# Kernel tuning notes

Hardware: AMD Instinct MI355X
Metric: run time of the kernel (lower is better)

The kernel has to match this reference:

```python
import jax, jax.numpy as jnp
import numpy as np

DIM = 256   # state dimension
T = 8192    # number of time steps
B = 32      # batch of initial conditions
DT = 0.01   # time-grid spacing


def make_A(dim):
    # Faithful to MagnusLadder.__init__: diag=-0.1, superdiag=+0.5, subdiag=-0.5
    A = np.zeros((dim, dim), dtype=np.float32)
    np.fill_diagonal(A, -0.1)
    idx = np.arange(dim - 1)
    A[idx, idx + 1] = 0.5
    A[idx + 1, idx] = -0.5
    return jnp.asarray(A)


def setup_inputs() -> dict:
    key = jax.random.key(0)
    x0 = jax.random.normal(key, (DIM, B), dtype=jnp.float32)
    t = jnp.arange(T, dtype=jnp.float32) * DT  # uniform time grid, dt = DT
    A = make_A(DIM)
    return {"t": t, "x0": x0, "A": A}


def reference(t, x0, A):
    dt = t[1] - t[0]
    expAdt = jax.scipy.linalg.expm(A * dt)  # [dim, dim]

    def step(x, _):
        x = expAdt @ x  # [dim, B]
        return x, x

    _, traj = jax.lax.scan(step, x0, None, length=T - 1)  # [T-1, dim, B]
    return jnp.concatenate([x0[None], traj], axis=0)       # [T, dim, B]
```

## Files before the change

### kernel.cpp

```cpp
#include <hip/hip_runtime.h>
#include <hip/hip_bf16.h>


#define DIMN 256
#define BB   32
#define TSTEPS 8192
#define KT   32
#define DTF  0.01f

typedef __attribute__((ext_vector_type(8))) short bf16x8;
typedef __attribute__((ext_vector_type(4))) float f32x4;

static __device__ __forceinline__ short f2bf(float f) {
    union { __hip_bfloat16 h; short s; } u;
    u.h = __float2bfloat16(f);
    return u.s;
}

__global__ __launch_bounds__(256) void k1_prep(const float* __restrict__ x0,
                                               unsigned short* __restrict__ vfold,
                                               float* __restrict__ yr,
                                               float* __restrict__ yi) {
    const float PI257 = (float)(3.14159265358979323846 / 257.0);
    const float S257  = sqrtf(2.0f / 257.0f);
    const int g = blockIdx.x;
    const int t = threadIdx.x;

    __shared__ float x0s[256 * 32];
    __shared__ float ve[256], vo[256];
    __shared__ float psr[8][32], psi[8][32];

    if (g < 256) {
        const int j = g, J = j >> 1, p = j & 1, m = t;
        const int n = ((j + 1) * (m + 1)) % 514;
        const float v = S257 * sinf((float)n * PI257);
        float sgn;
        if (p == 0) sgn = (J & 1) ? -1.f : 1.f;
        else        sgn = (J & 1) ?  1.f : -1.f;
        vfold[p * 32768 + J * 256 + m] = (unsigned short)f2bf(sgn * v);
    } else {
        const int m = g - 256;
        for (int idx = t; idx < 256 * 32; idx += 256) x0s[idx] = x0[idx];
        const int n = ((m + 1) * (t + 1)) % 514;
        const float v = S257 * sinf((float)n * PI257);
        const int j = t;
        float veJ = 0.f, voJ = 0.f;
        if ((j & 1) == 0) veJ = ((j & 3) == 0) ? v : -v;
        else              voJ = ((j & 3) == 3) ? v : -v;
        ve[j] = veJ; vo[j] = voJ;
        __syncthreads();
        const int b = t & 31, jg = t >> 5;
        float sr = 0.f, si = 0.f;
#pragma unroll
        for (int jj2 = 0; jj2 < 32; ++jj2) {
            const int jj = jg * 32 + jj2;
            sr += ve[jj] * x0s[jj * 32 + b];
            si += vo[jj] * x0s[jj * 32 + b];
        }
        psr[jg][b] = sr; psi[jg][b] = si;
        __syncthreads();
        if (t < 32) {
            float asr = 0.f, asi = 0.f;
#pragma unroll
            for (int q = 0; q < 8; ++q) { asr += psr[q][t]; asi += psi[q][t]; }
            yr[m * 32 + t] = asr;
            yi[m * 32 + t] = asi;
        }
    }
}

__global__ __launch_bounds__(512, 2) void k2_main(const unsigned short* __restrict__ vfold,
                                                  const float* __restrict__ yr,
                                                  const float* __restrict__ yi,
                                                  float* __restrict__ out) {
    __shared__ unsigned short ubuf[2][2][2][8192];
    const float PI257   = (float)(3.14159265358979323846 / 257.0);
    const float INV2PI  = (float)(1.0 / (2.0 * 3.14159265358979323846));
    const int tid  = threadIdx.x;
    const int lane = tid & 63;
    const int wave = tid >> 6;
    const int k0   = blockIdx.x * KT;

    const int bA   = tid & 15;
    const int mblk = tid >> 4;
    const int m0   = mblk << 3;

    float threv[8], yrv0[8], yiv0[8], yrv1[8], yiv1[8];
#pragma unroll
    for (int i = 0; i < 8; ++i) {
        const int m = m0 + i;
        const float lam = cosf((float)(m + 1) * PI257);
        threv[i] = DTF * lam * INV2PI;
        yrv0[i] = yr[m * 32 + bA];       yiv0[i] = yi[m * 32 + bA];
        yrv1[i] = yr[m * 32 + bA + 16];  yiv1[i] = yi[m * 32 + bA + 16];
    }
    const int ksA = m0 >> 5, gA2 = (m0 >> 3) & 3;
    const int wOff0 = bA * 256        + (((ksA ^ (bA & 7)))        << 3) + (gA2 << 6);
    const int wOff1 = (bA + 16) * 256 + (((ksA ^ ((bA + 16) & 7))) << 3) + (gA2 << 6);

    const int p  = wave & 1;
    const int nt = (wave >> 1) & 1;
    const int rh = wave >> 2;
    const int rA = lane & 15;
    const int gA = lane >> 4;
    bf16x8 afr[4][8];
#pragma unroll
    for (int rt = 0; rt < 4; ++rt) {
        const unsigned short* arow =
            vfold + p * 32768 + (rh * 64 + rt * 16 + rA) * 256 + gA * 8;
#pragma unroll
        for (int ks = 0; ks < 8; ++ks)
            afr[rt][ks] = *reinterpret_cast<const bf16x8*>(arow + ks * 32);
    }
    const int brd   = nt * 16 + rA;
    const int h     = brd & 7;
    const int rbase = brd * 256 + (gA << 6);

    float dec = expf(-0.001f * (float)k0);
    const float decr = expf(-0.001f);

    for (int r = 0; r < KT / 2; ++r) {
        const int d = r & 1;
#pragma unroll
        for (int kw = 0; kw < 2; ++kw) {
            const float kf = (float)(k0 + 2 * r + kw);
            bf16x8 vur0, vui0, vur1, vui1;
#pragma unroll
            for (int i = 0; i < 8; ++i) {
                const float ang = kf * threv[i];
                const float fr  = ang - floorf(ang);
                const float c   = __builtin_amdgcn_cosf(fr);
                const float s   = __builtin_amdgcn_sinf(fr);
                vur0[i] = f2bf(c * yrv0[i] - s * yiv0[i]);
                vui0[i] = f2bf(c * yiv0[i] + s * yrv0[i]);
                vur1[i] = f2bf(c * yrv1[i] - s * yiv1[i]);
                vui1[i] = f2bf(c * yiv1[i] + s * yrv1[i]);
            }
            *reinterpret_cast<bf16x8*>(&ubuf[d][kw][0][wOff0]) = vur0;
            *reinterpret_cast<bf16x8*>(&ubuf[d][kw][1][wOff0]) = vui0;
            *reinterpret_cast<bf16x8*>(&ubuf[d][kw][0][wOff1]) = vur1;
            *reinterpret_cast<bf16x8*>(&ubuf[d][kw][1][wOff1]) = vui1;
        }
        __syncthreads();

#pragma unroll
        for (int kw = 0; kw < 2; ++kw) {
            const unsigned short* up = &ubuf[d][kw][p][0];
            float* outk = out + (size_t)(k0 + 2 * r + kw) * 8192;
            f32x4 acc[4];
#pragma unroll
            for (int rt = 0; rt < 4; ++rt) acc[rt] = (f32x4){0.f, 0.f, 0.f, 0.f};
#pragma unroll
            for (int ks = 0; ks < 8; ++ks) {
                const bf16x8 bfr =
                    *reinterpret_cast<const bf16x8*>(up + rbase + ((ks ^ h) << 3));
#pragma unroll
                for (int rt = 0; rt < 4; ++rt)
                    acc[rt] = __builtin_amdgcn_mfma_f32_16x16x32_bf16(
                        afr[rt][ks], bfr, acc[rt], 0, 0, 0);
            }
#pragma unroll
            for (int rt = 0; rt < 4; ++rt) {
#pragma unroll
                for (int q = 0; q < 4; ++q) {
                    const int j = 2 * (rh * 64 + rt * 16 + gA * 4 + q) + p;
                    outk[j * 32 + brd] = acc[rt][q] * dec;
                }
            }
            dec *= decr;
        }
    }
}

extern "C" void kernel_launch(void* const* d_in, const int* in_sizes, int n_in,
                              void* d_out, int out_size, void* d_ws, size_t ws_size,
                              hipStream_t stream) {
    const float* x0 = (const float*)d_in[1];
    float* out = (float*)d_out;

    unsigned short* vfold = (unsigned short*)d_ws;
    float* yr = (float*)((char*)d_ws + 131072);
    float* yi = (float*)((char*)d_ws + 131072 + 32768);

    k1_prep<<<512, 256, 0, stream>>>(x0, vfold, yr, yi);
    k2_main<<<256, 512, 0, stream>>>(vfold, yr, yi, out);
}
```

Measured before the change: 272.8 us.

## Swap MFMA operand roles so output stores become contiguous float4 writes

Transposes the MFMA formulation: the folded eigenvector matrix is now held in registers as the B operand, and the per-step coefficient tile from shared memory becomes the A operand. Each wave now covers a 32x32 output block (2x2 tiles) instead of 64x16, so its accumulators hold four consecutive batch entries per lane and can be written as 16-byte vector stores rather than scattered scalar stores. The LDS swizzle for writing and reading the coefficient buffer is changed to match. The goal is better coalescing of the large output write stream, in exchange for two LDS fragment loads per k-step instead of one.

Result: no change. 274.4 us (+0.6%).

```diff
diff --git a/kernel.cpp b/kernel.cpp
--- a/kernel.cpp
+++ b/kernel.cpp
@@ -94,27 +94,25 @@
         yrv0[i] = yr[m * 32 + bA];       yiv0[i] = yi[m * 32 + bA];
         yrv1[i] = yr[m * 32 + bA + 16];  yiv1[i] = yi[m * 32 + bA + 16];
     }
-    const int ksA = m0 >> 5, gA2 = (m0 >> 3) & 3;
-    const int wOff0 = bA * 256        + (((ksA ^ (bA & 7)))        << 3) + (gA2 << 6);
-    const int wOff1 = (bA + 16) * 256 + (((ksA ^ ((bA + 16) & 7))) << 3) + (gA2 << 6);
+    const int C0    = (mblk & 24) + ((mblk ^ (bA & 7)) & 7);
+    const int wOff0 = bA * 256 + C0 * 8;
+    const int wOff1 = wOff0 + 16 * 256;
 
     const int p  = wave & 1;
-    const int nt = (wave >> 1) & 1;
-    const int rh = wave >> 2;
+    const int wp = wave >> 1;
     const int rA = lane & 15;
     const int gA = lane >> 4;
-    bf16x8 afr[4][8];
+    const int rl7 = rA & 7;
+
+    bf16x8 bfrv[2][8];
 #pragma unroll
-    for (int rt = 0; rt < 4; ++rt) {
-        const unsigned short* arow =
-            vfold + p * 32768 + (rh * 64 + rt * 16 + rA) * 256 + gA * 8;
+    for (int ntile = 0; ntile < 2; ++ntile) {
+        const unsigned short* vrow =
+            vfold + p * 32768 + (wp * 32 + ntile * 16 + rA) * 256 + gA * 8;
 #pragma unroll
         for (int ks = 0; ks < 8; ++ks)
-            afr[rt][ks] = *reinterpret_cast<const bf16x8*>(arow + ks * 32);
+            bfrv[ntile][ks] = *reinterpret_cast<const bf16x8*>(vrow + ks * 32);
     }
-    const int brd   = nt * 16 + rA;
-    const int h     = brd & 7;
-    const int rbase = brd * 256 + (gA << 6);
 
     float dec = expf(-0.001f * (float)k0);
     const float decr = expf(-0.001f);
@@ -147,24 +145,35 @@
         for (int kw = 0; kw < 2; ++kw) {
             const unsigned short* up = &ubuf[d][kw][p][0];
             float* outk = out + (size_t)(k0 + 2 * r + kw) * 8192;
-            f32x4 acc[4];
+            f32x4 acc[2][2];
 #pragma unroll
-            for (int rt = 0; rt < 4; ++rt) acc[rt] = (f32x4){0.f, 0.f, 0.f, 0.f};
+            for (int mt = 0; mt < 2; ++mt)
+#pragma unroll
+                for (int ntile = 0; ntile < 2; ++ntile)
+                    acc[mt][ntile] = (f32x4){0.f, 0.f, 0.f, 0.f};
 #pragma unroll
             for (int ks = 0; ks < 8; ++ks) {
-                const bf16x8 bfr =
-                    *reinterpret_cast<const bf16x8*>(up + rbase + ((ks ^ h) << 3));
+                const int mo = ks * 4 + gA;
+                const int csw = (mo & 24) + ((mo ^ rl7) & 7);
 #pragma unroll
-                for (int rt = 0; rt < 4; ++rt)
-                    acc[rt] = __builtin_amdgcn_mfma_f32_16x16x32_bf16(
-                        afr[rt][ks], bfr, acc[rt], 0, 0, 0);
+                for (int mt = 0; mt < 2; ++mt) {
+                    const bf16x8 afr = *reinterpret_cast<const bf16x8*>(
+                        up + (mt * 16 + rA) * 256 + csw * 8);
+#pragma unroll
+                    for (int ntile = 0; ntile < 2; ++ntile)
+                        acc[mt][ntile] = __builtin_amdgcn_mfma_f32_16x16x32_bf16(
+                            afr, bfrv[ntile][ks], acc[mt][ntile], 0, 0, 0);
+                }
             }
 #pragma unroll
-            for (int rt = 0; rt < 4; ++rt) {
+            for (int ntile = 0; ntile < 2; ++ntile) {
+                const int j = 2 * (wp * 32 + ntile * 16 + rA) + p;
 #pragma unroll
-                for (int q = 0; q < 4; ++q) {
-                    const int j = 2 * (rh * 64 + rt * 16 + gA * 4 + q) + p;
-                    outk[j * 32 + brd] = acc[rt][q] * dec;
+                for (int mt = 0; mt < 2; ++mt) {
+                    f32x4 v4;
+#pragma unroll
+                    for (int q = 0; q < 4; ++q) v4[q] = acc[mt][ntile][q] * dec;
+                    *reinterpret_cast<f32x4*>(&outk[j * 32 + mt * 16 + gA * 4]) = v4;
                 }
             }
             dec *= decr;
```
